# Optimization experiments

Measured on AMD Instinct MI355X. Metric: run time of the kernel, lower is better.

Reference implementation:

```python
import jax, jax.numpy as jnp
import numpy as np

B, NBC, H, W, HID, OUT = 4, 128, 64, 64, 64, 1
NINT = H * W

def _lin_init(key, fan_in, fan_out):
    kw, kb = jax.random.split(key)
    bound = 1.0 / np.sqrt(fan_in)
    w = jax.random.uniform(kw, (fan_in, fan_out), minval=-bound, maxval=bound, dtype=jnp.float32)
    b = jax.random.uniform(kb, (fan_out,), minval=-bound, maxval=bound, dtype=jnp.float32)
    return w, b

def setup_inputs() -> dict:
    key = jax.random.key(0)
    ks = jax.random.split(key, 7)
    boundary_info = jax.random.normal(ks[0], (B, NBC, 3), dtype=jnp.float32)
    interior_coords = jax.random.uniform(ks[1], (B, NINT, 2), minval=-1.0, maxval=1.0, dtype=jnp.float32)
    W0, b0 = _lin_init(ks[2], 3, HID)        # boundary_encoder layer 0
    W1, b1 = _lin_init(ks[3], HID, HID)      # boundary_encoder layer 1
    G0w, G0b = _lin_init(ks[4], HID + 2, HID)  # green_kernel layer 0
    G1w, G1b = _lin_init(ks[5], HID, HID)      # green_kernel layer 1
    G2w, G2b = _lin_init(ks[6], HID, OUT)      # green_kernel layer 2
    return {"boundary_info": boundary_info, "interior_coords": interior_coords,
            "W0": W0, "b0": b0, "W1": W1, "b1": b1,
            "G0w": G0w, "G0b": G0b, "G1w": G1w, "G1b": G1b,
            "G2w": G2w, "G2b": G2b,
            "interior_h": H, "interior_w": W}

def reference(boundary_info, interior_coords, W0, b0, W1, b1,
              G0w, G0b, G1w, G1b, G2w, G2b, interior_h, interior_w):
    batch, n_bc, _ = boundary_info.shape
    hid = W0.shape[1]
    # boundary encoder: (B, NBC, HID)
    bf = jax.nn.relu(boundary_info @ W0 + b0)
    bf = jax.nn.relu(bf @ W1 + b1)
    # green kernel layer 0: split weight over concat([bf, coords]) so the
    # concatenated (B,NBC,NINT,HID+2) tensor is never materialized.
    a = bf @ G0w[:hid]                      # (B, NBC, HID)
    c = interior_coords @ G0w[hid:]         # (B, NINT, HID)
    h1 = jax.nn.relu(a[:, :, None, :] + c[:, None, :, :] + G0b)  # (B,NBC,NINT,HID)
    h2 = jax.nn.relu(h1 @ G1w + G1b)        # (B, NBC, NINT, HID)
    contribution = h2 @ G2w + G2b           # (B, NBC, NINT, OUT)
    u = contribution.sum(axis=1) / n_bc     # (B, NINT, OUT)
    return u.reshape(batch, 1, interior_h, interior_w)
```

## Files before the change

### kernel.cpp

```cpp
#include <hip/hip_runtime.h>
#include <hip/hip_bf16.h>

#define BB   4
#define NBC  128
#define NINT 4096
#define HID  64

using short8  = __attribute__((ext_vector_type(8)))  short;
using float4v = __attribute__((ext_vector_type(4)))  float;
using f2      = __attribute__((ext_vector_type(2)))  float;
using int4v   = __attribute__((ext_vector_type(4)))  int;

static __device__ __forceinline__ short f2bf(float f) {
    __hip_bfloat16 h = __float2bfloat16(f);
    return __builtin_bit_cast(short, h);
}
static __device__ __forceinline__ unsigned fbits(float f) {
    return __builtin_bit_cast(unsigned, f);
}
static __device__ __forceinline__ unsigned pack_bf_trunc(float lo, float hi) {
    return __builtin_amdgcn_perm(fbits(hi), fbits(lo), 0x07060302u);
}

__global__ void __launch_bounds__(256) bge_prep(
    const float* __restrict__ binfo,
    const float* __restrict__ W0,
    const float* __restrict__ b0,
    const float* __restrict__ W1,
    const float* __restrict__ b1,
    const float* __restrict__ G0w,
    const float* __restrict__ G0b,
    float* __restrict__ aprime,
    float* __restrict__ out)
{
    __shared__ float sW1[HID * HID];
    __shared__ float sG0[HID * HID];
    __shared__ float shv [4][HID];
    __shared__ float shv2[4][HID];

    const int tid = threadIdx.x;
    const int wv  = tid >> 6;
    const int t   = tid & 63;
    const int row = blockIdx.x * 4 + wv;

    const int g = blockIdx.x * 256 + tid;
    if (g < BB * NINT) out[g] = 0.0f;

    for (int idx = tid; idx < HID * HID / 4; idx += 256) {
        ((float4*)sW1)[idx] = ((const float4*)W1)[idx];
        ((float4*)sG0)[idx] = ((const float4*)G0w)[idx];
    }

    const float x0 = binfo[row*3+0];
    const float x1 = binfo[row*3+1];
    const float x2 = binfo[row*3+2];
    float h = fmaxf(x0*W0[t] + x1*W0[64+t] + x2*W0[128+t] + b0[t], 0.0f);
    shv[wv][t] = h;
    __syncthreads();

    float acc = b1[t];
    #pragma unroll 8
    for (int k = 0; k < HID; ++k) acc += shv[wv][k] * sW1[k*64 + t];
    shv2[wv][t] = fmaxf(acc, 0.0f);
    __syncthreads();

    float a = G0b[t];
    #pragma unroll 8
    for (int k = 0; k < HID; ++k) a += shv2[wv][k] * sG0[k*64 + t];
    aprime[row*HID + t] = a;
}

__global__ void __launch_bounds__(256, 2) bge_main(
    const float* __restrict__ icoord,
    const float* __restrict__ G0w,
    const float* __restrict__ G1w,
    const float* __restrict__ G1b,
    const float* __restrict__ G2w,
    const float* __restrict__ G2b,
    const float* __restrict__ aprime,
    float* __restrict__ out)
{
    __shared__ float sred[4][32];

    const int b    = blockIdx.y;
    const int i0   = blockIdx.x * 32;
    const int zh   = blockIdx.z;
    const int tid  = threadIdx.x;
    const int wv   = tid >> 6;
    const int lane = tid & 63;
    const int ln   = lane & 15;
    const int q    = lane >> 4;

    const float2 cc0 = ((const float2*)icoord)[(size_t)b*NINT + i0 + ln];
    const float2 cc1 = ((const float2*)icoord)[(size_t)b*NINT + i0 + 16 + ln];

    f2 cre[2][2][4];
    #pragma unroll
    for (int kh = 0; kh < 2; ++kh)
        #pragma unroll
        for (int jj = 0; jj < 8; ++jj) {
            const int k = kh*32 + q*8 + jj;
            const float gx = G0w[64*64 + k], gy = G0w[65*64 + k];
            cre[0][kh][jj>>1][jj&1] = cc0.x*gx + cc0.y*gy;
            cre[1][kh][jj>>1][jj&1] = cc1.x*gx + cc1.y*gy;
        }

    short8 bfrag[2][4];
    #pragma unroll
    for (int kh = 0; kh < 2; ++kh)
        #pragma unroll
        for (int nt = 0; nt < 4; ++nt)
            #pragma unroll
            for (int jj = 0; jj < 8; ++jj)
                bfrag[kh][nt][jj] = f2bf(G1w[(kh*32 + q*8 + jj)*64 + nt*16 + ln]);

    float nb1[4], g2v[4];
    float corr = 0.0f;
    #pragma unroll
    for (int nt = 0; nt < 4; ++nt) {
        const float bv = G1b[nt*16 + ln];
        const float gv = G2w[nt*16 + ln];
        nb1[nt] = -bv;  g2v[nt] = gv;  corr += bv * gv;
    }

    f2 s[2][2];
    s[0][0] = (f2)0.0f; s[0][1] = (f2)0.0f; s[1][0] = (f2)0.0f; s[1][1] = (f2)0.0f;
    const float4v zc4 = (float4v)0.0f;

    const float* arow = aprime + ((size_t)b*NBC + zh*64 + wv*16)*HID;
    #pragma unroll 1
    for (int it = 0; it < 16; ++it, arow += HID) {
        short8 af[2][2];
        #pragma unroll
        for (int kh = 0; kh < 2; ++kh) {
            const float4 v0 = *(const float4*)(arow + kh*32 + q*8);
            const float4 v1 = *(const float4*)(arow + kh*32 + q*8 + 4);
            f2 w[4];
            w[0][0]=v0.x; w[0][1]=v0.y; w[1][0]=v0.z; w[1][1]=v0.w;
            w[2][0]=v1.x; w[2][1]=v1.y; w[3][0]=v1.z; w[3][1]=v1.w;
            #pragma unroll
            for (int ih = 0; ih < 2; ++ih) {
                const f2 e0 = w[0] + cre[ih][kh][0];
                const f2 e1 = w[1] + cre[ih][kh][1];
                const f2 e2 = w[2] + cre[ih][kh][2];
                const f2 e3 = w[3] + cre[ih][kh][3];
                int4v di;
                di[0] = (int)pack_bf_trunc(fmaxf(e0[0],0.f), fmaxf(e0[1],0.f));
                di[1] = (int)pack_bf_trunc(fmaxf(e1[0],0.f), fmaxf(e1[1],0.f));
                di[2] = (int)pack_bf_trunc(fmaxf(e2[0],0.f), fmaxf(e2[1],0.f));
                di[3] = (int)pack_bf_trunc(fmaxf(e3[0],0.f), fmaxf(e3[1],0.f));
                af[ih][kh] = __builtin_bit_cast(short8, di);
            }
        }
        #pragma unroll
        for (int ih = 0; ih < 2; ++ih)
            #pragma unroll
            for (int nt = 0; nt < 4; ++nt) {
                float4v acc = __builtin_amdgcn_mfma_f32_16x16x32_bf16(
                                  af[ih][0], bfrag[0][nt], zc4, 0, 0, 0);
                acc = __builtin_amdgcn_mfma_f32_16x16x32_bf16(
                                  af[ih][1], bfrag[1][nt], acc, 0, 0, 0);
                f2 m0, m1;
                m0[0] = fmaxf(acc[0], nb1[nt]); m0[1] = fmaxf(acc[1], nb1[nt]);
                m1[0] = fmaxf(acc[2], nb1[nt]); m1[1] = fmaxf(acc[3], nb1[nt]);
                s[ih][0] += m0 * g2v[nt];
                s[ih][1] += m1 * g2v[nt];
            }
    }

    {
        const f2 cadd = (f2)(16.0f * corr);
        s[0][0] += cadd; s[0][1] += cadd; s[1][0] += cadd; s[1][1] += cadd;
    }

    float v8[8] = { s[0][0][0], s[0][0][1], s[0][1][0], s[0][1][1],
                    s[1][0][0], s[1][0][1], s[1][1][0], s[1][1][1] };
    #pragma unroll
    for (int t = 0; t < 8; ++t) {
        float v = v8[t];
        v += __shfl_xor(v, 1);
        v += __shfl_xor(v, 2);
        v += __shfl_xor(v, 4);
        v += __shfl_xor(v, 8);
        v8[t] = v;
    }
    if (ln == 0) {
        #pragma unroll
        for (int ih = 0; ih < 2; ++ih)
            #pragma unroll
            for (int r = 0; r < 4; ++r)
                sred[wv][ih*16 + q*4 + r] = v8[ih*4 + r];
    }
    __syncthreads();

    if (tid < 32) {
        const float tot = sred[0][tid] + sred[1][tid] + sred[2][tid] + sred[3][tid];
        atomicAdd(out + (size_t)b*NINT + i0 + tid,
                  tot * (1.0f/128.0f) + 0.5f * G2b[0]);
    }
}

extern "C" void kernel_launch(void* const* d_in, const int* in_sizes, int n_in,
                              void* d_out, int out_size, void* d_ws, size_t ws_size,
                              hipStream_t stream) {
    const float* binfo  = (const float*)d_in[0];
    const float* icoord = (const float*)d_in[1];
    const float* W0     = (const float*)d_in[2];
    const float* b0     = (const float*)d_in[3];
    const float* W1     = (const float*)d_in[4];
    const float* b1     = (const float*)d_in[5];
    const float* G0w    = (const float*)d_in[6];
    const float* G0b    = (const float*)d_in[7];
    const float* G1w    = (const float*)d_in[8];
    const float* G1b    = (const float*)d_in[9];
    const float* G2w    = (const float*)d_in[10];
    const float* G2b    = (const float*)d_in[11];

    float* aprime = (float*)d_ws;

    hipLaunchKernelGGL(bge_prep, dim3(BB*NBC/4), dim3(256), 0, stream,
                       binfo, W0, b0, W1, b1, G0w, G0b, aprime, (float*)d_out);
    hipLaunchKernelGGL(bge_main, dim3(NINT/32, BB, 2), dim3(256), 0, stream,
                       icoord, G0w, G1w, G1b, G2w, G2b, aprime,
                       (float*)d_out);
}
```

Baseline: 120.6 us.

## Split boundary reduction four ways and prefetch next aprime row

Splits the boundary-condition dimension across four z-blocks instead of two, so each wave handles 8 rows instead of 16. The grid doubles to 2048 blocks, and the bias-correction and G2b scaling factors are adjusted to match. Each loop iteration now loads the next aprime row into registers before the current row is used, which hides global load latency. It also uses packed vector max for the ReLUs and drops the occupancy hint from launch bounds. The costs are twice as many atomic adds on the output, repeated per-block setup of the G1w fragments and coordinate terms, and higher register pressure from the prefetch.

```diff
diff --git a/kernel.cpp b/kernel.cpp
--- a/kernel.cpp
+++ b/kernel.cpp
@@ -70,7 +70,7 @@
     aprime[row*HID + t] = a;
 }
 
-__global__ void __launch_bounds__(256, 2) bge_main(
+__global__ void __launch_bounds__(256) bge_main(
     const float* __restrict__ icoord,
     const float* __restrict__ G0w,
     const float* __restrict__ G1w,
@@ -84,7 +84,7 @@
 
     const int b    = blockIdx.y;
     const int i0   = blockIdx.x * 32;
-    const int zh   = blockIdx.z;
+    const int zq   = blockIdx.z;
     const int tid  = threadIdx.x;
     const int wv   = tid >> 6;
     const int lane = tid & 63;
@@ -127,31 +127,44 @@
     s[0][0] = (f2)0.0f; s[0][1] = (f2)0.0f; s[1][0] = (f2)0.0f; s[1][1] = (f2)0.0f;
     const float4v zc4 = (float4v)0.0f;
 
-    const float* arow = aprime + ((size_t)b*NBC + zh*64 + wv*16)*HID;
+    const float* ar = aprime + ((size_t)b*NBC + zq*32 + wv*8)*HID;
+
+    float4 cv00 = *(const float4*)(ar + q*8);
+    float4 cv01 = *(const float4*)(ar + q*8 + 4);
+    float4 cv10 = *(const float4*)(ar + 32 + q*8);
+    float4 cv11 = *(const float4*)(ar + 32 + q*8 + 4);
+
     #pragma unroll 1
-    for (int it = 0; it < 16; ++it, arow += HID) {
+    for (int it = 0; it < 8; ++it, ar += HID) {
+        const float* nr = ar + ((it < 7) ? HID : 0);
+        const float4 nv00 = *(const float4*)(nr + q*8);
+        const float4 nv01 = *(const float4*)(nr + q*8 + 4);
+        const float4 nv10 = *(const float4*)(nr + 32 + q*8);
+        const float4 nv11 = *(const float4*)(nr + 32 + q*8 + 4);
+
         short8 af[2][2];
         #pragma unroll
         for (int kh = 0; kh < 2; ++kh) {
-            const float4 v0 = *(const float4*)(arow + kh*32 + q*8);
-            const float4 v1 = *(const float4*)(arow + kh*32 + q*8 + 4);
+            const float4 v0 = kh ? cv10 : cv00;
+            const float4 v1 = kh ? cv11 : cv01;
             f2 w[4];
             w[0][0]=v0.x; w[0][1]=v0.y; w[1][0]=v0.z; w[1][1]=v0.w;
             w[2][0]=v1.x; w[2][1]=v1.y; w[3][0]=v1.z; w[3][1]=v1.w;
             #pragma unroll
             for (int ih = 0; ih < 2; ++ih) {
-                const f2 e0 = w[0] + cre[ih][kh][0];
-                const f2 e1 = w[1] + cre[ih][kh][1];
-                const f2 e2 = w[2] + cre[ih][kh][2];
-                const f2 e3 = w[3] + cre[ih][kh][3];
+                const f2 e0 = __builtin_elementwise_max(w[0] + cre[ih][kh][0], (f2)0.0f);
+                const f2 e1 = __builtin_elementwise_max(w[1] + cre[ih][kh][1], (f2)0.0f);
+                const f2 e2 = __builtin_elementwise_max(w[2] + cre[ih][kh][2], (f2)0.0f);
+                const f2 e3 = __builtin_elementwise_max(w[3] + cre[ih][kh][3], (f2)0.0f);
                 int4v di;
-                di[0] = (int)pack_bf_trunc(fmaxf(e0[0],0.f), fmaxf(e0[1],0.f));
-                di[1] = (int)pack_bf_trunc(fmaxf(e1[0],0.f), fmaxf(e1[1],0.f));
-                di[2] = (int)pack_bf_trunc(fmaxf(e2[0],0.f), fmaxf(e2[1],0.f));
-                di[3] = (int)pack_bf_trunc(fmaxf(e3[0],0.f), fmaxf(e3[1],0.f));
+                di[0] = (int)pack_bf_trunc(e0[0], e0[1]);
+                di[1] = (int)pack_bf_trunc(e1[0], e1[1]);
+                di[2] = (int)pack_bf_trunc(e2[0], e2[1]);
+                di[3] = (int)pack_bf_trunc(e3[0], e3[1]);
                 af[ih][kh] = __builtin_bit_cast(short8, di);
             }
         }
+
         #pragma unroll
         for (int ih = 0; ih < 2; ++ih)
             #pragma unroll
@@ -160,16 +173,19 @@
                                   af[ih][0], bfrag[0][nt], zc4, 0, 0, 0);
                 acc = __builtin_amdgcn_mfma_f32_16x16x32_bf16(
                                   af[ih][1], bfrag[1][nt], acc, 0, 0, 0);
-                f2 m0, m1;
-                m0[0] = fmaxf(acc[0], nb1[nt]); m0[1] = fmaxf(acc[1], nb1[nt]);
-                m1[0] = fmaxf(acc[2], nb1[nt]); m1[1] = fmaxf(acc[3], nb1[nt]);
-                s[ih][0] += m0 * g2v[nt];
-                s[ih][1] += m1 * g2v[nt];
+                f2 a01; a01[0] = acc[0]; a01[1] = acc[1];
+                f2 a23; a23[0] = acc[2]; a23[1] = acc[3];
+                a01 = __builtin_elementwise_max(a01, (f2)nb1[nt]);
+                a23 = __builtin_elementwise_max(a23, (f2)nb1[nt]);
+                s[ih][0] += a01 * g2v[nt];
+                s[ih][1] += a23 * g2v[nt];
             }
+
+        cv00 = nv00; cv01 = nv01; cv10 = nv10; cv11 = nv11;
     }
 
     {
-        const f2 cadd = (f2)(16.0f * corr);
+        const f2 cadd = (f2)(8.0f * corr);
         s[0][0] += cadd; s[0][1] += cadd; s[1][0] += cadd; s[1][1] += cadd;
     }
 
@@ -196,7 +212,7 @@
     if (tid < 32) {
         const float tot = sred[0][tid] + sred[1][tid] + sred[2][tid] + sred[3][tid];
         atomicAdd(out + (size_t)b*NINT + i0 + tid,
-                  tot * (1.0f/128.0f) + 0.5f * G2b[0]);
+                  tot * (1.0f/128.0f) + 0.25f * G2b[0]);
     }
 }
 
@@ -220,7 +236,7 @@
 
     hipLaunchKernelGGL(bge_prep, dim3(BB*NBC/4), dim3(256), 0, stream,
                        binfo, W0, b0, W1, b1, G0w, G0b, aprime, (float*)d_out);
-    hipLaunchKernelGGL(bge_main, dim3(NINT/32, BB, 2), dim3(256), 0, stream,
+    hipLaunchKernelGGL(bge_main, dim3(NINT/32, BB, 4), dim3(256), 0, stream,
                        icoord, G0w, G1w, G1b, G2w, G2b, aprime,
                        (float*)d_out);
 }
```

Result: faster. 116.1 us (-3.7%).
